# Kernel optimization log

Measured on AMD Instinct MI355X. Metric: run time of the kernel, lower is better.

## Reference

```python
import jax, jax.numpy as jnp
import numpy as np

B, S, D = 2, 2048, 1024
NH, HD = 16, 64
MLP = 4096
EPS = 1e-6  # flax nnx.RMSNorm default epsilon


def rms_norm(x, scale):
    var = jnp.mean(jnp.square(x.astype(jnp.float32)), axis=-1, keepdims=True)
    return (x * jax.lax.rsqrt(var + EPS)).astype(x.dtype) * scale


def setup_inputs() -> dict:
    key = jax.random.key(0)
    ks = jax.random.split(key, 16)
    lin = lambda k, fin, fout: jax.random.normal(k, (fin, fout), jnp.float32) / np.sqrt(fin)
    x = jax.random.normal(ks[0], (B, S, D), jnp.float32)
    # causal mask [b, s, s]
    mask = jnp.broadcast_to(jnp.tril(jnp.ones((S, S), jnp.bool_))[None], (B, S, S))
    return {
        "x": x,
        "mask": mask,
        "attn_norm_scale": jnp.ones((D,), jnp.float32),
        "q_w": lin(ks[1], D, D), "q_b": jnp.zeros((D,), jnp.float32),
        "k_w": lin(ks[2], D, D), "k_b": jnp.zeros((D,), jnp.float32),
        "v_w": lin(ks[3], D, D), "v_b": jnp.zeros((D,), jnp.float32),
        "o_w": lin(ks[4], D, D), "o_b": jnp.zeros((D,), jnp.float32),
        "ffn_norm_scale": jnp.ones((D,), jnp.float32),
        "gate_w": lin(ks[5], D, MLP), "gate_b": jnp.zeros((MLP,), jnp.float32),
        "up_w": lin(ks[6], D, MLP), "up_b": jnp.zeros((MLP,), jnp.float32),
        "down_w": lin(ks[7], MLP, D), "down_b": jnp.zeros((D,), jnp.float32),
    }


def reference(x, mask, attn_norm_scale, q_w, q_b, k_w, k_b, v_w, v_b, o_w, o_b,
              ffn_norm_scale, gate_w, gate_b, up_w, up_b, down_w, down_b):
    b, s, d = x.shape
    h = rms_norm(x, attn_norm_scale)
    q = (h @ q_w + q_b).reshape(b, s, NH, HD)
    k = (h @ k_w + k_b).reshape(b, s, NH, HD)
    v = (h @ v_w + v_b).reshape(b, s, NH, HD)
    scale = jnp.float32(HD) ** -0.5
    logits = jnp.einsum('bsnh,btnh->bnst', q, k) * scale  # [b, n, s, s]
    logits = jnp.where(mask[:, None, :, :], logits, jnp.finfo(logits.dtype).min)
    attn = jax.nn.softmax(logits.astype(jnp.float32), axis=-1).astype(x.dtype)
    attn_out = jnp.einsum('bnst,btnh->bsnh', attn, v).reshape(b, s, d)
    x = x + attn_out @ o_w + o_b
    h = rms_norm(x, ffn_norm_scale)
    ffn = (jax.nn.silu(h @ gate_w + gate_b) * (h @ up_w + up_b)) @ down_w + down_b
    return x + ffn
```

## Files before the change

kernel.cpp:

```cpp
#include <hip/hip_runtime.h>

#define S_LEN 2048
#define DMODEL 1024
#define NHEADS 16
#define MLPDIM 4096

typedef float f32x4 __attribute__((ext_vector_type(4)));
typedef __bf16 bf16x8 __attribute__((ext_vector_type(8)));
typedef __bf16 bf16x4 __attribute__((ext_vector_type(4)));

__device__ __forceinline__ void gload_lds16(const void* gsrc, void* ldst) {
  __builtin_amdgcn_global_load_lds(
      (const __attribute__((address_space(1))) void*)gsrc,
      (__attribute__((address_space(3))) void*)ldst, 16, 0, 0);
}

#define BARR() __builtin_amdgcn_s_barrier()
#define VMC(n) do { asm volatile("s_waitcnt vmcnt(" #n ")" ::: "memory"); __builtin_amdgcn_sched_barrier(0); } while (0)

__global__ __launch_bounds__(256) void transpose_cast64_k(
    const float* __restrict__ in, __bf16* __restrict__ out, int K, int N) {
  __shared__ __bf16 tile[64][66];
  int n0 = blockIdx.x * 64, k0 = blockIdx.y * 64;
  int t = threadIdx.x;
  int rr = (t & 63) >> 4, sl = t & 15, wv = t >> 6;
#pragma unroll
  for (int j = 0; j < 4; ++j) {
    int r = wv * 4 + rr + j * 16;
    f32x4 v = *(const f32x4*)(in + (size_t)(k0 + r) * N + n0 + sl * 4);
#pragma unroll
    for (int e = 0; e < 4; ++e) tile[r][sl * 4 + e] = (__bf16)v[e];
  }
  __syncthreads();
#pragma unroll
  for (int j = 0; j < 2; ++j) {
    int u = t + j * 256;
    int n = u >> 3, kc = u & 7;
    bf16x8 o;
#pragma unroll
    for (int e = 0; e < 8; ++e) o[e] = tile[kc * 8 + e][n];
    *(bf16x8*)(out + (size_t)(n0 + n) * K + k0 + kc * 8) = o;
  }
}

__global__ __launch_bounds__(256) void vtrans_k(
    const __bf16* __restrict__ qkv, __bf16* __restrict__ vt) {
  __shared__ __bf16 tile[32][33];
  int s0 = blockIdx.x * 32, c0 = blockIdx.y * 32, b = blockIdx.z;
  int tx = threadIdx.x & 31, ty = threadIdx.x >> 5;
#pragma unroll
  for (int r = 0; r < 32; r += 8)
    tile[r + ty][tx] = qkv[(size_t)(b * S_LEN + s0 + r + ty) * 3072 + 2048 + c0 + tx];
  __syncthreads();
#pragma unroll
  for (int r = 0; r < 32; r += 8)
    vt[(size_t)(b * 1024 + c0 + r + ty) * S_LEN + s0 + tx] = tile[tx][r + ty];
}

__global__ __launch_bounds__(256) void concat3_k(
    const float* __restrict__ a, const float* __restrict__ b,
    const float* __restrict__ c, float* __restrict__ dst) {
  int i = blockIdx.x * 256 + threadIdx.x;
  if (i < 1024) dst[i] = a[i];
  else if (i < 2048) dst[i] = b[i - 1024];
  else if (i < 3072) dst[i] = c[i - 2048];
}

__global__ __launch_bounds__(256) void rmsnorm_k(
    const float* __restrict__ x, const float* __restrict__ scale,
    __bf16* __restrict__ out) {
  int row = blockIdx.x, tid = threadIdx.x;
  f32x4 v = ((const f32x4*)(x + (size_t)row * DMODEL))[tid];
  float ss = v[0] * v[0] + v[1] * v[1] + v[2] * v[2] + v[3] * v[3];
#pragma unroll
  for (int off = 1; off < 64; off <<= 1) ss += __shfl_xor(ss, off, 64);
  __shared__ float part[4];
  if ((tid & 63) == 0) part[tid >> 6] = ss;
  __syncthreads();
  float tot = part[0] + part[1] + part[2] + part[3];
  float r = rsqrtf(tot * (1.0f / DMODEL) + 1e-6f);
  f32x4 s4 = ((const f32x4*)scale)[tid];
  bf16x4 o;
#pragma unroll
  for (int e = 0; e < 4; ++e) o[e] = (__bf16)(v[e] * r * s4[e]);
  ((bf16x4*)out)[(size_t)row * (DMODEL / 4) + tid] = o;
}

__global__ __launch_bounds__(256, 2) void gemm_gu(
    const __bf16* __restrict__ A, const __bf16* __restrict__ Gt,
    const __bf16* __restrict__ Ut, const float* __restrict__ gb,
    const float* __restrict__ ub, __bf16* __restrict__ Cout,
    int M, int N, int K) {
  __shared__ __attribute__((aligned(16))) __bf16 As[2][128 * 64];
  __shared__ __attribute__((aligned(16))) __bf16 Gs[2][64 * 64];
  __shared__ __attribute__((aligned(16))) __bf16 Us[2][64 * 64];
  int tid = threadIdx.x, lane = tid & 63, wave = tid >> 6;
  int l15 = lane & 15, g4 = lane >> 4;
  int lin = blockIdx.x;
  int xcd = lin & 7, idx = lin >> 3;
  int bxl = idx >> 4, byl = idx & 15;
  int bn = ((xcd & 3) * 16 + bxl) * 64;
  int bm = ((xcd >> 2) * 16 + byl) * 128;
  int wr = wave >> 1, wc = wave & 1;
  f32x4 ag[4][2] = {}, au[4][2] = {};
  const __bf16* Abase = A + (size_t)bm * K;
  const __bf16* Gbase = Gt + (size_t)bn * K;
  const __bf16* Ubase = Ut + (size_t)bn * K;

  auto stage = [&](int k0, int sb) {
#pragma unroll
    for (int j = 0; j < 4; ++j) {
      int u = tid + j * 256;
      int r = u >> 3, c = (u & 7) ^ (r & 7);
      gload_lds16(Abase + (size_t)r * K + k0 + c * 8, As[sb] + u * 8);
    }
#pragma unroll
    for (int j = 0; j < 2; ++j) {
      int u = tid + j * 256;
      int r = u >> 3, c = (u & 7) ^ (r & 7);
      gload_lds16(Gbase + (size_t)r * K + k0 + c * 8, Gs[sb] + u * 8);
      gload_lds16(Ubase + (size_t)r * K + k0 + c * 8, Us[sb] + u * 8);
    }
  };

  int NT = K >> 6;
  stage(0, 0);
  for (int t = 0; t < NT; ++t) {
    int sb = t & 1;
    if (t + 1 < NT) { stage((t + 1) << 6, sb ^ 1); VMC(8); }
    else { VMC(0); }
    BARR();
#pragma unroll
    for (int ks = 0; ks < 2; ++ks) {
      bf16x8 af[4], gf[2], uf[2];
#pragma unroll
      for (int m = 0; m < 4; ++m) {
        int r = wr * 64 + m * 16 + l15;
        af[m] = *(const bf16x8*)(As[sb] + r * 64 + (((4 * ks + g4) ^ (r & 7)) << 3));
      }
#pragma unroll
      for (int n = 0; n < 2; ++n) {
        int r = wc * 32 + n * 16 + l15;
        int off = r * 64 + (((4 * ks + g4) ^ (r & 7)) << 3);
        gf[n] = *(const bf16x8*)(Gs[sb] + off);
        uf[n] = *(const bf16x8*)(Us[sb] + off);
      }
      __builtin_amdgcn_s_setprio(1);
#pragma unroll
      for (int m = 0; m < 4; ++m)
#pragma unroll
        for (int n = 0; n < 2; ++n) {
          ag[m][n] = __builtin_amdgcn_mfma_f32_16x16x32_bf16(af[m], gf[n], ag[m][n], 0, 0, 0);
          au[m][n] = __builtin_amdgcn_mfma_f32_16x16x32_bf16(af[m], uf[n], au[m][n], 0, 0, 0);
        }
      __builtin_amdgcn_s_setprio(0);
    }
    BARR();
  }
  int r0 = bm + wr * 64 + g4 * 4;
  int c0 = bn + wc * 32 + l15;
#pragma unroll
  for (int n = 0; n < 2; ++n) {
    int c = c0 + n * 16;
    float gbv = gb[c], ubv = ub[c];
#pragma unroll
    for (int m = 0; m < 4; ++m) {
      int rb = r0 + m * 16;
#pragma unroll
      for (int rg = 0; rg < 4; ++rg) {
        float g = ag[m][n][rg] + gbv;
        float u = au[m][n][rg] + ubv;
        float v = g / (1.0f + __expf(-g)) * u;
        Cout[(size_t)(rb + rg) * N + c] = (__bf16)v;
      }
    }
  }
}

template <int OUT_BF16, int RESID, int SILU>
__global__ __launch_bounds__(256, 3) void gemm_n64(
    const __bf16* __restrict__ A, const __bf16* __restrict__ Bt,
    const float* __restrict__ bias, const float* __restrict__ resid,
    const __bf16* __restrict__ aux, void* __restrict__ Cout,
    int M, int N, int K) {
  __shared__ __attribute__((aligned(16))) __bf16 As[2][128 * 64];
  __shared__ __attribute__((aligned(16))) __bf16 Bs[2][64 * 64];
  int tid = threadIdx.x, lane = tid & 63, wave = tid >> 6;
  int l15 = lane & 15, g4 = lane >> 4;
  int npx = M >> 10;
  int xcd = blockIdx.x & 7, j = blockIdx.x >> 3;
  int bm = (xcd * npx + (j % npx)) * 128;
  int bn = (j / npx) * 64;
  int wr = wave >> 1, wc = wave & 1;
  f32x4 acc[4][2] = {};
  const __bf16* Abase = A + (size_t)bm * K;
  const __bf16* Bbase = Bt + (size_t)bn * K;

  auto stage = [&](int k0, int sb) {
#pragma unroll
    for (int i = 0; i < 4; ++i) {
      int u = tid + i * 256;
      int r = u >> 3, c = (u & 7) ^ (r & 7);
      gload_lds16(Abase + (size_t)r * K + k0 + c * 8, As[sb] + u * 8);
    }
#pragma unroll
    for (int i = 0; i < 2; ++i) {
      int u = tid + i * 256;
      int r = u >> 3, c = (u & 7) ^ (r & 7);
      gload_lds16(Bbase + (size_t)r * K + k0 + c * 8, Bs[sb] + u * 8);
    }
  };

  int NT = K >> 6;
  stage(0, 0);
  for (int t = 0; t < NT; ++t) {
    int sb = t & 1;
    if (t + 1 < NT) { stage((t + 1) << 6, sb ^ 1); VMC(6); }
    else { VMC(0); }
    BARR();
#pragma unroll
    for (int ks = 0; ks < 2; ++ks) {
      bf16x8 af[4], bfr[2];
#pragma unroll
      for (int m = 0; m < 4; ++m) {
        int r = wr * 64 + m * 16 + l15;
        af[m] = *(const bf16x8*)(As[sb] + r * 64 + (((4 * ks + g4) ^ (r & 7)) << 3));
      }
#pragma unroll
      for (int n = 0; n < 2; ++n) {
        int r = wc * 32 + n * 16 + l15;
        bfr[n] = *(const bf16x8*)(Bs[sb] + r * 64 + (((4 * ks + g4) ^ (r & 7)) << 3));
      }
      __builtin_amdgcn_s_setprio(1);
#pragma unroll
      for (int m = 0; m < 4; ++m)
#pragma unroll
        for (int n = 0; n < 2; ++n)
          acc[m][n] = __builtin_amdgcn_mfma_f32_16x16x32_bf16(af[m], bfr[n], acc[m][n], 0, 0, 0);
      __builtin_amdgcn_s_setprio(0);
    }
    BARR();
  }
  int r0 = bm + wr * 64 + g4 * 4;
  int c0 = bn + wc * 32 + l15;
#pragma unroll
  for (int n = 0; n < 2; ++n) {
    int c = c0 + n * 16;
    float bv = bias[c];
#pragma unroll
    for (int m = 0; m < 4; ++m) {
      int rb = r0 + m * 16;
#pragma unroll
      for (int rg = 0; rg < 4; ++rg) {
        int r = rb + rg;
        size_t idx = (size_t)r * N + c;
        float v = acc[m][n][rg] + bv;
        if (SILU) {
          float gg = (float)aux[idx];
          v *= gg / (1.0f + __expf(-gg));
        }
        if (RESID) v += resid[idx];
        if (OUT_BF16) ((__bf16*)Cout)[idx] = (__bf16)v;
        else ((float*)Cout)[idx] = v;
      }
    }
  }
}

#define SCL2E 0.180336879f
__global__ __launch_bounds__(512, 4) void attn_k(
    const __bf16* __restrict__ qkv, const __bf16* __restrict__ vt,
    __bf16* __restrict__ ao) {
  __shared__ __attribute__((aligned(16))) __bf16 Ks[2][128 * 64];
  __shared__ __attribute__((aligned(16))) __bf16 Vs[2][64 * 128];
  int tid = threadIdx.x, lane = tid & 63, w = tid >> 6;
  int l15 = lane & 15, g4 = lane >> 4;
  int bh = blockIdx.x, b = bh >> 4, h = bh & 15;
  int qt = 15 - blockIdx.y;
  int qb = qt * 128;
  int qw = qb + w * 16;
  const __bf16* qkvb = qkv + (size_t)b * S_LEN * 3072 + h * 64;
  const __bf16* kgb = qkvb + 1024;
  const __bf16* vtb = vt + (size_t)b * 1024 * S_LEN + (size_t)(h * 64) * S_LEN;

  bf16x8 qf[2];
#pragma unroll
  for (int ks = 0; ks < 2; ++ks)
    qf[ks] = *(const bf16x8*)(qkvb + (size_t)(qw + l15) * 3072 + 32 * ks + 8 * g4);

  f32x4 oa[4] = {};
  float mrow = -1e30f, lrow = 0.f;
  int q = qw + l15;
  int nt = qt + 1;

  auto stage = [&](int kvb, int buf) {
#pragma unroll
    for (int i = 0; i < 2; ++i) {
      int u = tid + i * 512;
      int r = u >> 3, c = u & 7;
      gload_lds16(kgb + (size_t)(kvb + r) * 3072 + ((c ^ (r & 7)) << 3),
                  Ks[buf] + w * 512 + i * 4096);
    }
#pragma unroll
    for (int i = 0; i < 2; ++i) {
      int u = tid + i * 512;
      int r = u >> 4, cu = u & 15;
      gload_lds16(vtb + (size_t)r * S_LEN + kvb + ((cu ^ (r & 7)) << 3),
                  Vs[buf] + w * 512 + i * 4096);
    }
  };

  stage(0, 0);
  __syncthreads();
  int buf = 0;
  for (int t = 0; t < nt; ++t) {
    int kvb = t * 128;
    if (t + 1 < nt) stage(kvb + 128, buf ^ 1);

    f32x4 sa[8];
#pragma unroll
    for (int i = 0; i < 8; ++i) sa[i] = f32x4{0.f, 0.f, 0.f, 0.f};
#pragma unroll
    for (int st = 0; st < 2; ++st)
#pragma unroll
      for (int ks = 0; ks < 2; ++ks) {
        bf16x8 kf[4];
#pragma unroll
        for (int n = 0; n < 4; ++n) {
          int rr = st * 64 + n * 16 + l15;
          int bc = (64 * ks + 16 * g4) ^ ((rr & 7) << 4);
          kf[n] = *(const bf16x8*)((const char*)Ks[buf] + rr * 128 + bc);
        }
        __builtin_amdgcn_s_setprio(1);
#pragma unroll
        for (int n = 0; n < 4; ++n)
          sa[st * 4 + n] = __builtin_amdgcn_mfma_f32_16x16x32_bf16(kf[n], qf[ks], sa[st * 4 + n], 0, 0, 0);
        __builtin_amdgcn_s_setprio(0);
      }

    bool lastt = (t == nt - 1);
    float nmx = -1e30f;
#pragma unroll
    for (int i = 0; i < 8; ++i)
#pragma unroll
      for (int rg = 0; rg < 4; ++rg) {
        float s = sa[i][rg] * SCL2E;
        if (lastt) {
          int key = kvb + (i >> 2) * 64 + (i & 3) * 16 + 4 * g4 + rg;
          s = (key <= q) ? s : -1e30f;
        }
        sa[i][rg] = s;
        nmx = fmaxf(nmx, s);
      }
    nmx = fmaxf(nmx, __shfl_xor(nmx, 16));
    nmx = fmaxf(nmx, __shfl_xor(nmx, 32));
    float nm = fmaxf(mrow, nmx);
    float sc = exp2f(mrow - nm);
    mrow = nm;
    float rs = 0.f;
    bf16x8 pa[2][2];
#pragma unroll
    for (int st = 0; st < 2; ++st)
#pragma unroll
      for (int ks = 0; ks < 2; ++ks)
#pragma unroll
        for (int hf = 0; hf < 2; ++hf)
#pragma unroll
          for (int rg = 0; rg < 4; ++rg) {
            float p = exp2f(sa[st * 4 + 2 * ks + hf][rg] - nm);
            rs += p;
            pa[st][ks][hf * 4 + rg] = (__bf16)p;
          }
    rs += __shfl_xor(rs, 16);
    rs += __shfl_xor(rs, 32);
    lrow = lrow * sc + rs;
#pragma unroll
    for (int rg = 0; rg < 4; ++rg) {
      float scq = __shfl(sc, 4 * g4 + rg);
#pragma unroll
      for (int dn = 0; dn < 4; ++dn) oa[dn][rg] *= scq;
    }

#pragma unroll
    for (int st = 0; st < 2; ++st)
#pragma unroll
      for (int ks = 0; ks < 2; ++ks) {
        __builtin_amdgcn_s_setprio(1);
#pragma unroll
        for (int dn = 0; dn < 4; ++dn) {
          int rr = dn * 16 + l15;
          int swz = (rr & 7) << 4;
          int bb = st * 128 + 64 * ks + 8 * g4;
          const char* vrow = (const char*)Vs[buf] + rr * 256;
          bf16x4 v0 = *(const bf16x4*)(vrow + (bb ^ swz));
          bf16x4 v1 = *(const bf16x4*)(vrow + ((bb + 32) ^ swz));
          bf16x8 vf;
          vf[0] = v0[0]; vf[1] = v0[1]; vf[2] = v0[2]; vf[3] = v0[3];
          vf[4] = v1[0]; vf[5] = v1[1]; vf[6] = v1[2]; vf[7] = v1[3];
          oa[dn] = __builtin_amdgcn_mfma_f32_16x16x32_bf16(pa[st][ks], vf, oa[dn], 0, 0, 0);
        }
        __builtin_amdgcn_s_setprio(0);
      }
    __syncthreads();
    buf ^= 1;
  }

  __bf16* aobase = ao + (size_t)b * S_LEN * DMODEL + h * 64;
#pragma unroll
  for (int rg = 0; rg < 4; ++rg) {
    float rl = 1.0f / __shfl(lrow, 4 * g4 + rg);
    int qo = qw + 4 * g4 + rg;
#pragma unroll
    for (int dn = 0; dn < 4; ++dn)
      aobase[(size_t)qo * DMODEL + dn * 16 + l15] = (__bf16)(oa[dn][rg] * rl);
  }
}

#define OFF_WQKV 0
#define OFF_WO 6291456
#define OFF_WG 8388608
#define OFF_WU 16777216
#define OFF_WD 25165824
#define OFF_BQKV 33554432
#define OFF_H 33570816
#define OFF_QKV 41959424
#define OFF_AO 67125248
#define OFF_T 75513856
#define OFF_VT OFF_T
#define OFF_X2 109068288

extern "C" void kernel_launch(void* const* d_in, const int* in_sizes, int n_in,
                              void* d_out, int out_size, void* d_ws, size_t ws_size,
                              hipStream_t stream) {
  (void)in_sizes; (void)n_in; (void)out_size; (void)ws_size;
  const float* x = (const float*)d_in[0];
  const float* attn_scale = (const float*)d_in[2];
  const float* q_w = (const float*)d_in[3];
  const float* q_b = (const float*)d_in[4];
  const float* k_w = (const float*)d_in[5];
  const float* k_b = (const float*)d_in[6];
  const float* v_w = (const float*)d_in[7];
  const float* v_b = (const float*)d_in[8];
  const float* o_w = (const float*)d_in[9];
  const float* o_b = (const float*)d_in[10];
  const float* ffn_scale = (const float*)d_in[11];
  const float* gate_w = (const float*)d_in[12];
  const float* gate_b = (const float*)d_in[13];
  const float* up_w = (const float*)d_in[14];
  const float* up_b = (const float*)d_in[15];
  const float* down_w = (const float*)d_in[16];
  const float* down_b = (const float*)d_in[17];

  char* ws = (char*)d_ws;
  __bf16* wqkv = (__bf16*)(ws + OFF_WQKV);
  __bf16* wo = (__bf16*)(ws + OFF_WO);
  __bf16* wg = (__bf16*)(ws + OFF_WG);
  __bf16* wu = (__bf16*)(ws + OFF_WU);
  __bf16* wd = (__bf16*)(ws + OFF_WD);
  float* bqkv = (float*)(ws + OFF_BQKV);
  __bf16* hbuf = (__bf16*)(ws + OFF_H);
  __bf16* qkvbuf = (__bf16*)(ws + OFF_QKV);
  __bf16* aobuf = (__bf16*)(ws + OFF_AO);
  __bf16* tbuf = (__bf16*)(ws + OFF_T);
  __bf16* vtbuf = (__bf16*)(ws + OFF_VT);
  float* x2 = (float*)(ws + OFF_X2);

  dim3 blk(256);
  transpose_cast64_k<<<dim3(16, 16), blk, 0, stream>>>(q_w, wqkv, 1024, 1024);
  transpose_cast64_k<<<dim3(16, 16), blk, 0, stream>>>(k_w, wqkv + 1024 * 1024, 1024, 1024);
  transpose_cast64_k<<<dim3(16, 16), blk, 0, stream>>>(v_w, wqkv + 2 * 1024 * 1024, 1024, 1024);
  transpose_cast64_k<<<dim3(16, 16), blk, 0, stream>>>(o_w, wo, 1024, 1024);
  transpose_cast64_k<<<dim3(64, 16), blk, 0, stream>>>(gate_w, wg, 1024, 4096);
  transpose_cast64_k<<<dim3(64, 16), blk, 0, stream>>>(up_w, wu, 1024, 4096);
  transpose_cast64_k<<<dim3(16, 64), blk, 0, stream>>>(down_w, wd, 4096, 1024);
  concat3_k<<<12, blk, 0, stream>>>(q_b, k_b, v_b, bqkv);
  rmsnorm_k<<<4096, blk, 0, stream>>>(x, attn_scale, hbuf);
  gemm_n64<1, 0, 0><<<dim3(1536), blk, 0, stream>>>(hbuf, wqkv, bqkv, nullptr, nullptr, qkvbuf, 4096, 3072, 1024);
  vtrans_k<<<dim3(64, 32, 2), blk, 0, stream>>>(qkvbuf, vtbuf);
  attn_k<<<dim3(32, 16), dim3(512), 0, stream>>>(qkvbuf, vtbuf, aobuf);
  gemm_n64<0, 1, 0><<<dim3(512), blk, 0, stream>>>(aobuf, wo, o_b, x, nullptr, x2, 4096, 1024, 1024);
  rmsnorm_k<<<4096, blk, 0, stream>>>(x2, ffn_scale, hbuf);
  gemm_gu<<<dim3(2048), blk, 0, stream>>>(hbuf, wg, wu, gate_b, up_b, tbuf, 4096, 4096, 1024);
  gemm_n64<0, 1, 0><<<dim3(512), blk, 0, stream>>>(tbuf, wd, down_b, x2, nullptr, (float*)d_out, 4096, 1024, 4096);
}
```

Baseline: 284.0 us.

## Replace double-buffered LDS pipeline in gate/up GEMM with single buffer, raise occupancy

The gate/up fused GEMM drops its double-buffered LDS prefetch pipeline in favour of a single-buffered load-sync-compute loop. The launch bounds hint moves from 2 to 4 blocks per CU. The intent is to halve LDS use and allow more resident blocks, so latency is hidden by other waves rather than by software prefetch. The cost is that global loads no longer overlap with MFMA work inside a block, and register pressure is capped more tightly.

```diff
diff --git a/kernel.cpp b/kernel.cpp
--- a/kernel.cpp
+++ b/kernel.cpp
@@ -86,14 +86,14 @@
   ((bf16x4*)out)[(size_t)row * (DMODEL / 4) + tid] = o;
 }
 
-__global__ __launch_bounds__(256, 2) void gemm_gu(
+__global__ __launch_bounds__(256, 4) void gemm_gu(
     const __bf16* __restrict__ A, const __bf16* __restrict__ Gt,
     const __bf16* __restrict__ Ut, const float* __restrict__ gb,
     const float* __restrict__ ub, __bf16* __restrict__ Cout,
     int M, int N, int K) {
-  __shared__ __attribute__((aligned(16))) __bf16 As[2][128 * 64];
-  __shared__ __attribute__((aligned(16))) __bf16 Gs[2][64 * 64];
-  __shared__ __attribute__((aligned(16))) __bf16 Us[2][64 * 64];
+  __shared__ __attribute__((aligned(16))) __bf16 As[128 * 64];
+  __shared__ __attribute__((aligned(16))) __bf16 Gs[64 * 64];
+  __shared__ __attribute__((aligned(16))) __bf16 Us[64 * 64];
   int tid = threadIdx.x, lane = tid & 63, wave = tid >> 6;
   int l15 = lane & 15, g4 = lane >> 4;
   int lin = blockIdx.x;
@@ -107,43 +107,35 @@
   const __bf16* Gbase = Gt + (size_t)bn * K;
   const __bf16* Ubase = Ut + (size_t)bn * K;
 
-  auto stage = [&](int k0, int sb) {
+  for (int k0 = 0; k0 < K; k0 += 64) {
 #pragma unroll
     for (int j = 0; j < 4; ++j) {
       int u = tid + j * 256;
       int r = u >> 3, c = (u & 7) ^ (r & 7);
-      gload_lds16(Abase + (size_t)r * K + k0 + c * 8, As[sb] + u * 8);
+      gload_lds16(Abase + (size_t)r * K + k0 + c * 8, As + u * 8);
     }
 #pragma unroll
     for (int j = 0; j < 2; ++j) {
       int u = tid + j * 256;
       int r = u >> 3, c = (u & 7) ^ (r & 7);
-      gload_lds16(Gbase + (size_t)r * K + k0 + c * 8, Gs[sb] + u * 8);
-      gload_lds16(Ubase + (size_t)r * K + k0 + c * 8, Us[sb] + u * 8);
-    }
-  };
-
-  int NT = K >> 6;
-  stage(0, 0);
-  for (int t = 0; t < NT; ++t) {
-    int sb = t & 1;
-    if (t + 1 < NT) { stage((t + 1) << 6, sb ^ 1); VMC(8); }
-    else { VMC(0); }
-    BARR();
+      gload_lds16(Gbase + (size_t)r * K + k0 + c * 8, Gs + u * 8);
+      gload_lds16(Ubase + (size_t)r * K + k0 + c * 8, Us + u * 8);
+    }
+    __syncthreads();
 #pragma unroll
     for (int ks = 0; ks < 2; ++ks) {
       bf16x8 af[4], gf[2], uf[2];
 #pragma unroll
       for (int m = 0; m < 4; ++m) {
         int r = wr * 64 + m * 16 + l15;
-        af[m] = *(const bf16x8*)(As[sb] + r * 64 + (((4 * ks + g4) ^ (r & 7)) << 3));
+        af[m] = *(const bf16x8*)(As + r * 64 + (((4 * ks + g4) ^ (r & 7)) << 3));
       }
 #pragma unroll
       for (int n = 0; n < 2; ++n) {
         int r = wc * 32 + n * 16 + l15;
         int off = r * 64 + (((4 * ks + g4) ^ (r & 7)) << 3);
-        gf[n] = *(const bf16x8*)(Gs[sb] + off);
-        uf[n] = *(const bf16x8*)(Us[sb] + off);
+        gf[n] = *(const bf16x8*)(Gs + off);
+        uf[n] = *(const bf16x8*)(Us + off);
       }
       __builtin_amdgcn_s_setprio(1);
 #pragma unroll
@@ -155,7 +147,7 @@
         }
       __builtin_amdgcn_s_setprio(0);
     }
-    BARR();
+    __syncthreads();
   }
   int r0 = bm + wr * 64 + g4 * 4;
   int c0 = bn + wc * 32 + l15;
```

Result: faster. 271.4 us (-4.4%).
